# Optimization experiments

Measured on AMD Instinct MI355X. Metric: run time of the kernel, lower is better.

The kernel has to match this reference:

```python
import jax, jax.numpy as jnp
import numpy as np

THETA = 0.5  # forward default arg
ALPHA = 0.2  # LeakyReLU negative slope
NEG_INF = -9e15


def setup_inputs() -> dict:
    key = jax.random.key(0)
    k1, k2, k3, k4, k5 = jax.random.split(key, 5)
    N, F_IN, F_OUT = 8192, 256, 256
    h = jax.random.normal(k1, (N, F_IN), dtype=jnp.float32)
    adj = jax.random.randint(k2, (N, N), 0, 2, dtype=jnp.int32)
    cv_values = jax.random.uniform(k3, (N,), dtype=jnp.float32)
    # xavier_uniform with gain=1.414
    g = 1.414
    bw = g * np.sqrt(6.0 / (F_IN + F_OUT))
    W = jax.random.uniform(k4, (F_IN, F_OUT), dtype=jnp.float32, minval=-bw, maxval=bw)
    ba = g * np.sqrt(6.0 / (2 * F_OUT + 1))
    a = jax.random.uniform(k5, (2 * F_OUT, 1), dtype=jnp.float32, minval=-ba, maxval=ba)
    return {"h": h, "adj": adj, "cv_values": cv_values, "W": W, "a": a}


def reference(h, adj, cv_values, W, a):
    # Wh: [N, F_out]
    Wh = h @ W
    F_out = Wh.shape[1]
    a1 = a[:F_out, 0]   # [F_out]
    a2 = a[F_out:, 0]   # [F_out]
    # e_ij = LeakyReLU([Wh_i ; Wh_j] . a) = LeakyReLU(Wh_i.a1 + Wh_j.a2)
    f1 = Wh @ a1        # [N]
    f2 = Wh @ a2        # [N]
    e = jax.nn.leaky_relu(f1[:, None] + f2[None, :], negative_slope=ALPHA)
    # CV bias: theta * cv_i broadcast across row i
    e = e + THETA * cv_values[:, None]
    att = jnp.where(adj > 0, e, jnp.float32(NEG_INF))
    att = jax.nn.softmax(att, axis=1)
    # dropout is identity in eval mode (training=False)
    h_prime = att @ Wh  # [N, F_out]
    return jax.nn.elu(h_prime)  # concat=True branch
```

## Files before the change

### kernel.cpp

```cpp
#include <hip/hip_runtime.h>
#include <cstdint>
#include <cstddef>

typedef _Float16 half8 __attribute__((ext_vector_type(8)));
typedef _Float16 half4 __attribute__((ext_vector_type(4)));
typedef float f32x4 __attribute__((ext_vector_type(4)));

#define GAT_N 8192
#define GAT_F 256
#define GAT_NW 256
#define GAT_NQ 8
#define GAT_ALPHA 0.2f
#define GAT_LOG2E 1.4426950408889634f

__device__ inline unsigned enc_f32(float x) {
    unsigned b = __float_as_uint(x);
    return (b & 0x80000000u) ? ~b : (b | 0x80000000u);
}
__device__ inline float dec_f32(unsigned u) {
    unsigned b = (u & 0x80000000u) ? (u ^ 0x80000000u) : ~u;
    return __uint_as_float(b);
}


__global__ __launch_bounds__(256) void gat_k0_pack(
    const int* __restrict__ adj, unsigned char* __restrict__ adjB)
{
    const int wv = threadIdx.x >> 6;
    const int lane = threadIdx.x & 63;
    const int row = blockIdx.x * 4 + wv;
    const int* src = adj + (size_t)row * GAT_N;
    unsigned char* dst = adjB + (size_t)row * (GAT_N / 8);
    #pragma unroll 4
    for (int k = 0; k < 16; ++k) {
        const int4 v0 = *reinterpret_cast<const int4*>(src + k * 512 + lane * 8);
        const int4 v1 = *reinterpret_cast<const int4*>(src + k * 512 + lane * 8 + 4);
        unsigned m = (unsigned)(v0.x > 0)        | ((unsigned)(v0.y > 0) << 1)
                   | ((unsigned)(v0.z > 0) << 2) | ((unsigned)(v0.w > 0) << 3)
                   | ((unsigned)(v1.x > 0) << 4) | ((unsigned)(v1.y > 0) << 5)
                   | ((unsigned)(v1.z > 0) << 6) | ((unsigned)(v1.w > 0) << 7);
        dst[k * 64 + lane] = (unsigned char)m;
    }
}

__global__ __launch_bounds__(256) void gat_k0b_convert(
    const float* __restrict__ W, _Float16* __restrict__ WT,
    unsigned* __restrict__ f2mxEnc)
{
    const int g = blockIdx.x * 256 + threadIdx.x;
    if (g == 0) *f2mxEnc = 0u;
    const int k = g >> 8, n = g & 255;
    WT[n * GAT_F + k] = (_Float16)W[g];
}

__global__ __launch_bounds__(256, 2) void gat_k1_gemm(
    const float* __restrict__ h, const _Float16* __restrict__ WT,
    const float* __restrict__ a, _Float16* __restrict__ whT2,
    float* __restrict__ f1L, float* __restrict__ f2L,
    unsigned* __restrict__ f2mxEnc)
{
    __shared__ float sP1[4][16], sP2[4][16];
    const int wv = threadIdx.x >> 6;
    const int lane = threadIdx.x & 63;
    const int l15 = lane & 15;
    const int quad = lane >> 4;
    const int r0 = blockIdx.x * 16;

    f32x4 acc[4];
    #pragma unroll
    for (int t = 0; t < 4; ++t) { f32x4 z = {0.f,0.f,0.f,0.f}; acc[t] = z; }

    #pragma unroll
    for (int k0 = 0; k0 < GAT_F; k0 += 32) {
        const float* ap = h + (size_t)(r0 + l15) * GAT_F + k0 + quad * 8;
        const float4 a0 = *reinterpret_cast<const float4*>(ap);
        const float4 a1 = *reinterpret_cast<const float4*>(ap + 4);
        half8 af;
        af[0] = (_Float16)a0.x; af[1] = (_Float16)a0.y;
        af[2] = (_Float16)a0.z; af[3] = (_Float16)a0.w;
        af[4] = (_Float16)a1.x; af[5] = (_Float16)a1.y;
        af[6] = (_Float16)a1.z; af[7] = (_Float16)a1.w;
        #pragma unroll
        for (int t = 0; t < 4; ++t) {
            half8 bf = *reinterpret_cast<const half8*>(
                WT + (size_t)(wv * 64 + t * 16 + l15) * GAT_F + k0 + quad * 8);
            acc[t] = __builtin_amdgcn_mfma_f32_16x16x32_f16(af, bf, acc[t], 0, 0, 0);
        }
    }

    float p1[4] = {0.f,0.f,0.f,0.f}, p2[4] = {0.f,0.f,0.f,0.f};
    #pragma unroll
    for (int t = 0; t < 4; ++t) {
        float a1c = a[wv * 64 + t * 16 + l15];
        float a2c = a[GAT_F + wv * 64 + t * 16 + l15];
        #pragma unroll
        for (int r = 0; r < 4; ++r) {
            p1[r] = fmaf(acc[t][r], a1c, p1[r]);
            p2[r] = fmaf(acc[t][r], a2c, p2[r]);
        }
    }
    #pragma unroll
    for (int off = 1; off < 16; off <<= 1) {
        #pragma unroll
        for (int r = 0; r < 4; ++r) {
            p1[r] += __shfl_xor(p1[r], off);
            p2[r] += __shfl_xor(p2[r], off);
        }
    }
    if (l15 == 0) {
        #pragma unroll
        for (int r = 0; r < 4; ++r) {
            sP1[wv][quad * 4 + r] = p1[r];
            sP2[wv][quad * 4 + r] = p2[r];
        }
    }
    __syncthreads();
    if (threadIdx.x < 16) {
        const int row = threadIdx.x;
        const float s1 = (sP1[0][row] + sP1[1][row] + sP1[2][row] + sP1[3][row]) * GAT_LOG2E;
        const float s2 = (sP2[0][row] + sP2[1][row] + sP2[2][row] + sP2[3][row]) * GAT_LOG2E;
        f1L[r0 + row] = s1;
        f2L[r0 + row] = s2;
        float mx = s2;
        #pragma unroll
        for (int off = 1; off < 16; off <<= 1) mx = fmaxf(mx, __shfl_xor(mx, off));
        if (row == 0) atomicMax(f2mxEnc, enc_f32(mx));
    }

    const size_t tbase = (size_t)(r0 >> 6) * 16384
                       + (((r0 & 63) >> 3) + (quad >> 1)) * 2048
                       + (quad & 1) * 4;
    #pragma unroll
    for (int t = 0; t < 4; ++t) {
        const int c = wv * 64 + t * 16 + l15;
        half4 hv;
        #pragma unroll
        for (int r = 0; r < 4; ++r) hv[r] = (_Float16)acc[t][r];
        *reinterpret_cast<half4*>(whT2 + tbase + c * 8) = hv;
    }
}

__global__ __launch_bounds__(256, 2) void gat_k3_attn(
    const unsigned* __restrict__ adjW, const float* __restrict__ f1L,
    const float* __restrict__ f2L, const unsigned* __restrict__ f2mxEnc,
    const _Float16* __restrict__ whT2,
    _Float16* __restrict__ Ph,
    float* __restrict__ L)
{
    __shared__ __align__(16) _Float16 sB[2][16384];

    const int bx = blockIdx.x;
    const int q  = bx & 7;
    const int rb = bx >> 3;
    const int wv = threadIdx.x >> 6;
    const int lane = threadIdx.x & 63;
    const int l15 = lane & 15;
    const int quad = lane >> 4;

    const int kq = q * 1024;
    const int r0 = rb * 128 + wv * 32;
    const int rA = r0 + l15;
    const int rB = rA + 16;

    const float fmxL = dec_f32(*f2mxEnc);
    const float f1A = f1L[rA];
    const float f1B = f1L[rB];
    const float sA = f1A + fmxL;
    const float sBv = f1B + fmxL;
    const float CA = fmaxf(sA, GAT_ALPHA * sA);
    const float CB = fmaxf(sBv, GAT_ALPHA * sBv);
    const float uA = f1A - CA, vA = GAT_ALPHA * f1A - CA;
    const float uB = f1B - CB, vB = GAT_ALPHA * f1B - CB;

    f32x4 acc[2][16];
    #pragma unroll
    for (int s = 0; s < 2; ++s)
        #pragma unroll
        for (int t = 0; t < 16; ++t) {
            f32x4 z = {0.f,0.f,0.f,0.f};
            acc[s][t] = z;
        }
    float d0 = 0.f, d1 = 0.f;

    const uint2* awA = reinterpret_cast<const uint2*>(adjW + (size_t)rA * GAT_NW + q * 32);
    const uint2* awB = reinterpret_cast<const uint2*>(adjW + (size_t)rB * GAT_NW + q * 32);
    const float* f2q = f2L + kq + quad * 8;

    const _Float16* tile0 = whT2 + (size_t)(q * 16) * 16384 + (size_t)lane * 8;
    #define STAGE(buf, step)                                                   \
        {                                                                      \
            _Pragma("unroll")                                                  \
            for (int i = 0; i < 8; ++i) {                                      \
                const int off = wv * 4096 + i * 512;                           \
                const _Float16* gp = tile0 + (size_t)(step) * 16384 + off;     \
                _Float16* lp = &sB[buf][off];                                  \
                __builtin_amdgcn_global_load_lds(                              \
                    (const __attribute__((address_space(1))) void*)gp,         \
                    (__attribute__((address_space(3))) void*)lp, 16, 0, 0);    \
            }                                                                  \
        }

    uint2 nA = awA[0];
    uint2 nB = awB[0];
    float4 nfa = *reinterpret_cast<const float4*>(f2q);
    float4 nfb = *reinterpret_cast<const float4*>(f2q + 4);
    STAGE(0, 0)
    __syncthreads();

    for (int step = 0; step < 16; ++step) {
        const int cur = step & 1;
        const uint2 cA = nA, cB = nB;
        if (step < 15) {
            nA = awA[step + 1];
            nB = awB[step + 1];
            STAGE(1 - cur, step + 1)
        }

        #pragma unroll
        for (int k2 = 0; k2 < 2; ++k2) {
            const int u = step * 2 + k2;
            const float4 cfa = nfa, cfb = nfb;
            if (u < 31) {
                nfa = *reinterpret_cast<const float4*>(f2q + (u + 1) * 32);
                nfb = *reinterpret_cast<const float4*>(f2q + (u + 1) * 32 + 4);
            }
            const unsigned wA = k2 ? cA.y : cA.x;
            const unsigned wB = k2 ? cB.y : cB.x;
            const unsigned mA = (wA >> (quad * 8)) & 0xffu;
            const unsigned mB = (wB >> (quad * 8)) & 0xffu;
            const float f2v[8] = {cfa.x, cfa.y, cfa.z, cfa.w,
                                  cfb.x, cfb.y, cfb.z, cfb.w};
            float af2[8];
            #pragma unroll
            for (int j = 0; j < 8; ++j) af2[j] = GAT_ALPHA * f2v[j];

            half8 pA, pB;
            #pragma unroll
            for (int j = 0; j < 8; ++j) {
                float pa = __builtin_amdgcn_exp2f(fmaxf(uA + f2v[j], vA + af2[j]));
                pa = (mA & (1u << j)) ? pa : 0.f;
                d0 += pa;
                pA[j] = (_Float16)pa;
                float pb = __builtin_amdgcn_exp2f(fmaxf(uB + f2v[j], vB + af2[j]));
                pb = (mB & (1u << j)) ? pb : 0.f;
                d1 += pb;
                pB[j] = (_Float16)pb;
            }

            const int lbase = (k2 * 4 + quad) * 2048 + l15 * 8;
            #pragma unroll
            for (int t = 0; t < 16; ++t) {
                half8 bf = *reinterpret_cast<const half8*>(
                    &sB[cur][lbase + t * 128]);
                acc[0][t] = __builtin_amdgcn_mfma_f32_16x16x32_f16(pA, bf, acc[0][t], 0, 0, 0);
                acc[1][t] = __builtin_amdgcn_mfma_f32_16x16x32_f16(pB, bf, acc[1][t], 0, 0, 0);
            }
        }
        __syncthreads();
    }
    #undef STAGE

    d0 += __shfl_xor(d0, 16); d0 += __shfl_xor(d0, 32);
    d1 += __shfl_xor(d1, 16); d1 += __shfl_xor(d1, 32);
    if (lane < 16) {
        float* Lq = L + q * GAT_N;
        Lq[rA] = d0; Lq[rB] = d1;
    }

    const int wid = rb * 4 + wv;
    _Float16* Pq = Ph + ((size_t)q * 256 + wid) * 8192;
    #pragma unroll
    for (int s = 0; s < 2; ++s)
        #pragma unroll
        for (int t = 0; t < 16; ++t) {
            half4 hv;
            #pragma unroll
            for (int r = 0; r < 4; ++r) hv[r] = (_Float16)acc[s][t][r];
            *reinterpret_cast<half4*>(Pq + (size_t)(((s * 16 + t) * 64 + lane) * 4)) = hv;
        }
}

__global__ __launch_bounds__(256) void gat_k4_final(
    const _Float16* __restrict__ Ph, const float* __restrict__ L,
    float* __restrict__ out)
{
    const int tid = threadIdx.x;
    const int wid = blockIdx.x >> 3;
    __shared__ float s_rl[32];
    if (tid < 32) {
        const int row = wid * 32 + tid;
        float s = 0.f;
        #pragma unroll
        for (int q = 0; q < GAT_NQ; ++q) s += L[q * GAT_N + row];
        s_rl[tid] = 1.0f / fmaxf(s, 1e-30f);
    }
    __syncthreads();

    const int idx = blockIdx.x * 256 + tid;
    const int rem = idx & 2047;
    const int lane = rem & 63;
    const int st = rem >> 6;
    const int s = st >> 4, t = st & 15;
    const int l15 = lane & 15, quad = lane >> 4;
    const int lrow0 = s * 16 + quad * 4;
    const int col = t * 16 + l15;

    float accv[4] = {0.f, 0.f, 0.f, 0.f};
    #pragma unroll
    for (int q = 0; q < GAT_NQ; ++q) {
        half4 v = *reinterpret_cast<const half4*>(
            Ph + ((size_t)q * 256 + wid) * 8192 + (size_t)rem * 4);
        #pragma unroll
        for (int r = 0; r < 4; ++r) accv[r] += (float)v[r];
    }
    #pragma unroll
    for (int r = 0; r < 4; ++r) {
        const float v = accv[r] * s_rl[lrow0 + r];
        const float o = v > 0.f ? v : expm1f(v);
        out[(size_t)(wid * 32 + lrow0 + r) * GAT_F + col] = o;
    }
}

extern "C" void kernel_launch(void* const* d_in, const int* in_sizes, int n_in,
                              void* d_out, int out_size, void* d_ws, size_t ws_size,
                              hipStream_t stream)
{
    const float* h   = (const float*)d_in[0];
    const int*   adj = (const int*)d_in[1];
    const float* W   = (const float*)d_in[3];
    const float* a   = (const float*)d_in[4];
    float* out = (float*)d_out;
    char* ws = (char*)d_ws;

    const size_t SLAB = (size_t)GAT_N * GAT_F * 2;

    size_t off = 0;
    _Float16* whT2 = (_Float16*)(ws + off); off += SLAB;
    _Float16* Ph  = (_Float16*)(ws + off); off += GAT_NQ * SLAB;
    unsigned char* adjB = (unsigned char*)(ws + off); off += (size_t)GAT_N * GAT_N / 8;
    _Float16* WT  = (_Float16*)(ws + off); off += (size_t)GAT_F * GAT_F * 2;
    float* f1L = (float*)(ws + off); off += GAT_N * 4;
    float* f2L = (float*)(ws + off); off += GAT_N * 4;
    float* L   = (float*)(ws + off); off += GAT_NQ * GAT_N * 4;
    unsigned* f2mxEnc = (unsigned*)(ws + off); off += 256;

    gat_k0_pack<<<2048, 256, 0, stream>>>(adj, adjB);
    gat_k0b_convert<<<256, 256, 0, stream>>>(W, WT, f2mxEnc);
    gat_k1_gemm<<<512, 256, 0, stream>>>(h, WT, a, whT2, f1L, f2L, f2mxEnc);
    gat_k3_attn<<<512, 256, 0, stream>>>((const unsigned*)adjB, f1L, f2L, f2mxEnc, whT2, Ph, L);
    gat_k4_final<<<2048, 256, 0, stream>>>(Ph, L, out);
}
```

Measured before the change: 442.4 us.

## Fuse adjacency bit-packing into the attention kernel and drop the pack pass

Removes the separate kernel that packed the int32 adjacency matrix into bitmasks. The attention kernel now reads the int32 adjacency rows directly, prefetching one step ahead, and packs them into per-lane masks inside its pipelined loop. This saves one extra kernel launch plus the bitmask write and re-read. In exchange, the attention kernel streams 256MB of int32 data itself, which adds register pressure (eight int4 prefetch registers) and memory traffic to a kernel that is already heavy on MFMA work.

```diff
diff --git a/kernel.cpp b/kernel.cpp
--- a/kernel.cpp
+++ b/kernel.cpp
@@ -8,7 +8,6 @@
 
 #define GAT_N 8192
 #define GAT_F 256
-#define GAT_NW 256
 #define GAT_NQ 8
 #define GAT_ALPHA 0.2f
 #define GAT_LOG2E 1.4426950408889634f
@@ -22,26 +21,13 @@
     return __uint_as_float(b);
 }
 
-
-__global__ __launch_bounds__(256) void gat_k0_pack(
-    const int* __restrict__ adj, unsigned char* __restrict__ adjB)
-{
-    const int wv = threadIdx.x >> 6;
-    const int lane = threadIdx.x & 63;
-    const int row = blockIdx.x * 4 + wv;
-    const int* src = adj + (size_t)row * GAT_N;
-    unsigned char* dst = adjB + (size_t)row * (GAT_N / 8);
-    #pragma unroll 4
-    for (int k = 0; k < 16; ++k) {
-        const int4 v0 = *reinterpret_cast<const int4*>(src + k * 512 + lane * 8);
-        const int4 v1 = *reinterpret_cast<const int4*>(src + k * 512 + lane * 8 + 4);
-        unsigned m = (unsigned)(v0.x > 0)        | ((unsigned)(v0.y > 0) << 1)
-                   | ((unsigned)(v0.z > 0) << 2) | ((unsigned)(v0.w > 0) << 3)
-                   | ((unsigned)(v1.x > 0) << 4) | ((unsigned)(v1.y > 0) << 5)
-                   | ((unsigned)(v1.z > 0) << 6) | ((unsigned)(v1.w > 0) << 7);
-        dst[k * 64 + lane] = (unsigned char)m;
-    }
-}
+__device__ inline unsigned pack8(int4 v0, int4 v1) {
+    return (unsigned)(v0.x > 0)        | ((unsigned)(v0.y > 0) << 1)
+         | ((unsigned)(v0.z > 0) << 2) | ((unsigned)(v0.w > 0) << 3)
+         | ((unsigned)(v1.x > 0) << 4) | ((unsigned)(v1.y > 0) << 5)
+         | ((unsigned)(v1.z > 0) << 6) | ((unsigned)(v1.w > 0) << 7);
+}
+
 
 __global__ __launch_bounds__(256) void gat_k0b_convert(
     const float* __restrict__ W, _Float16* __restrict__ WT,
@@ -141,7 +127,7 @@
 }
 
 __global__ __launch_bounds__(256, 2) void gat_k3_attn(
-    const unsigned* __restrict__ adjW, const float* __restrict__ f1L,
+    const int* __restrict__ adj, const float* __restrict__ f1L,
     const float* __restrict__ f2L, const unsigned* __restrict__ f2mxEnc,
     const _Float16* __restrict__ whT2,
     _Float16* __restrict__ Ph,
@@ -182,9 +168,29 @@
         }
     float d0 = 0.f, d1 = 0.f;
 
-    const uint2* awA = reinterpret_cast<const uint2*>(adjW + (size_t)rA * GAT_NW + q * 32);
-    const uint2* awB = reinterpret_cast<const uint2*>(adjW + (size_t)rB * GAT_NW + q * 32);
+    const int* aprA = adj + (size_t)rA * GAT_N + kq + quad * 8;
+    const int* aprB = adj + (size_t)rB * GAT_N + kq + quad * 8;
     const float* f2q = f2L + kq + quad * 8;
+
+    int4 xA0, xA1, xA2, xA3, xB0, xB1, xB2, xB3;
+    #define ADJLOAD(s)                                                         \
+        {                                                                      \
+            const int* pa = aprA + (s) * 64;                                   \
+            const int* pb = aprB + (s) * 64;                                   \
+            xA0 = *reinterpret_cast<const int4*>(pa);                          \
+            xA1 = *reinterpret_cast<const int4*>(pa + 4);                      \
+            xA2 = *reinterpret_cast<const int4*>(pa + 32);                     \
+            xA3 = *reinterpret_cast<const int4*>(pa + 36);                     \
+            xB0 = *reinterpret_cast<const int4*>(pb);                          \
+            xB1 = *reinterpret_cast<const int4*>(pb + 4);                      \
+            xB2 = *reinterpret_cast<const int4*>(pb + 32);                     \
+            xB3 = *reinterpret_cast<const int4*>(pb + 36);                     \
+        }
+    #define ADJPACK(ma, mb)                                                    \
+        {                                                                      \
+            ma = pack8(xA0, xA1) | (pack8(xA2, xA3) << 8);                     \
+            mb = pack8(xB0, xB1) | (pack8(xB2, xB3) << 8);                     \
+        }
 
     const _Float16* tile0 = whT2 + (size_t)(q * 16) * 16384 + (size_t)lane * 8;
     #define STAGE(buf, step)                                                   \
@@ -200,19 +206,19 @@
             }                                                                  \
         }
 
-    uint2 nA = awA[0];
-    uint2 nB = awB[0];
+    ADJLOAD(0)
     float4 nfa = *reinterpret_cast<const float4*>(f2q);
     float4 nfb = *reinterpret_cast<const float4*>(f2q + 4);
     STAGE(0, 0)
+    unsigned cmA, cmB;
+    ADJPACK(cmA, cmB)
+    unsigned nmA = 0, nmB = 0;
     __syncthreads();
 
     for (int step = 0; step < 16; ++step) {
         const int cur = step & 1;
-        const uint2 cA = nA, cB = nB;
         if (step < 15) {
-            nA = awA[step + 1];
-            nB = awB[step + 1];
+            ADJLOAD(step + 1)
             STAGE(1 - cur, step + 1)
         }
 
@@ -224,10 +230,8 @@
                 nfa = *reinterpret_cast<const float4*>(f2q + (u + 1) * 32);
                 nfb = *reinterpret_cast<const float4*>(f2q + (u + 1) * 32 + 4);
             }
-            const unsigned wA = k2 ? cA.y : cA.x;
-            const unsigned wB = k2 ? cB.y : cB.x;
-            const unsigned mA = (wA >> (quad * 8)) & 0xffu;
-            const unsigned mB = (wB >> (quad * 8)) & 0xffu;
+            const unsigned mA = (cmA >> (k2 * 8)) & 0xffu;
+            const unsigned mB = (cmB >> (k2 * 8)) & 0xffu;
             const float f2v[8] = {cfa.x, cfa.y, cfa.z, cfa.w,
                                   cfb.x, cfb.y, cfb.z, cfb.w};
             float af2[8];
@@ -256,9 +260,13 @@
                 acc[1][t] = __builtin_amdgcn_mfma_f32_16x16x32_f16(pB, bf, acc[1][t], 0, 0, 0);
             }
         }
+        if (step < 15) ADJPACK(nmA, nmB)
         __syncthreads();
+        cmA = nmA; cmB = nmB;
     }
     #undef STAGE
+    #undef ADJLOAD
+    #undef ADJPACK
 
     d0 += __shfl_xor(d0, 16); d0 += __shfl_xor(d0, 32);
     d1 += __shfl_xor(d1, 16); d1 += __shfl_xor(d1, 32);
@@ -337,16 +345,14 @@
     size_t off = 0;
     _Float16* whT2 = (_Float16*)(ws + off); off += SLAB;
     _Float16* Ph  = (_Float16*)(ws + off); off += GAT_NQ * SLAB;
-    unsigned char* adjB = (unsigned char*)(ws + off); off += (size_t)GAT_N * GAT_N / 8;
     _Float16* WT  = (_Float16*)(ws + off); off += (size_t)GAT_F * GAT_F * 2;
     float* f1L = (float*)(ws + off); off += GAT_N * 4;
     float* f2L = (float*)(ws + off); off += GAT_N * 4;
     float* L   = (float*)(ws + off); off += GAT_NQ * GAT_N * 4;
     unsigned* f2mxEnc = (unsigned*)(ws + off); off += 256;
 
-    gat_k0_pack<<<2048, 256, 0, stream>>>(adj, adjB);
     gat_k0b_convert<<<256, 256, 0, stream>>>(W, WT, f2mxEnc);
     gat_k1_gemm<<<512, 256, 0, stream>>>(h, WT, a, whT2, f1L, f2L, f2mxEnc);
-    gat_k3_attn<<<512, 256, 0, stream>>>((const unsigned*)adjB, f1L, f2L, f2mxEnc, whT2, Ph, L);
+    gat_k3_attn<<<512, 256, 0, stream>>>(adj, f1L, f2L, f2mxEnc, whT2, Ph, L);
     gat_k4_final<<<2048, 256, 0, stream>>>(Ph, L, out);
 }
```

After: 430.1 us. 1.03x faster.
